# Kernel tuning notes

Measured on AMD Instinct MI355X. Metric: run time of the kernel, lower is better.

## Reference

```python
import jax, jax.numpy as jnp
import numpy as np
from math import factorial, comb

N_NODES = 50000
N_EDGES = 640000
FEAT = 32
NUM_BASIS = 8
CUTOFF = 5.0
MAX_Z = 118
NUM_ITERS = 3
LMAX = 2
K = (LMAX + 1) ** 2  # 9 spherical channels for max_degree=2


def _assoc_legendre(c, s, lmax):
    # associated Legendre P_l^m without Condon-Shortley phase
    P = {(0, 0): np.ones_like(c)}
    for m in range(1, lmax + 1):
        P[(m, m)] = P[(m - 1, m - 1)] * (2 * m - 1) * s
    for m in range(lmax):
        P[(m + 1, m)] = (2 * m + 1) * c * P[(m, m)]
    for m in range(lmax + 1):
        for l in range(m + 2, lmax + 1):
            P[(l, m)] = ((2 * l - 1) * c * P[(l - 1, m)] - (l + m - 1) * P[(l - 2, m)]) / (l - m)
    return P


def _real_sh_np(xyz, lmax):
    # Racah-normalized real spherical harmonics (Y_00 = 1), order m=-l..l
    r = np.linalg.norm(xyz, axis=1)
    cth = xyz[:, 2] / r
    sth = np.sqrt(np.maximum(1.0 - cth ** 2, 0.0))
    phi = np.arctan2(xyz[:, 1], xyz[:, 0])
    P = _assoc_legendre(cth, sth, lmax)
    cols = []
    for l in range(lmax + 1):
        for m in range(-l, l + 1):
            am = abs(m)
            if m == 0:
                cols.append(P[(l, 0)])
            else:
                nrm = np.sqrt(2.0 * factorial(l - am) / factorial(l + am))
                ang = np.cos(am * phi) if m > 0 else np.sin(am * phi)
                cols.append(nrm * P[(l, am)] * ang)
    return np.stack(cols, axis=1)


def _gaunt_tensor():
    # cg[k1,k2,k3]: expansion of Y_k1 * Y_k2 onto Y_k3 (degrees <= 2).
    # Products of degree<=2 harmonics lie exactly in span of degree<=4 harmonics,
    # so the least-squares fit below recovers exact coefficients.
    rng = np.random.default_rng(0)
    pts = rng.normal(size=(4096, 3))
    pts /= np.linalg.norm(pts, axis=1, keepdims=True)
    A = _real_sh_np(pts, 2 * LMAX)  # (M, 25)
    Y = A[:, :K]                    # (M, 9)
    prod = (Y[:, :, None] * Y[:, None, :]).reshape(len(pts), K * K)
    coef, *_ = np.linalg.lstsq(A, prod, rcond=None)  # (25, 81)
    return coef[:K].reshape(K, K, K).transpose(1, 2, 0).astype(np.float32)


CG = jnp.asarray(_gaunt_tensor())  # (9, 9, 9)
LOG_BINOM = jnp.asarray([np.log(comb(NUM_BASIS - 1, kk)) for kk in range(NUM_BASIS)], dtype=jnp.float32)


def _sh_l2(u):
    # Racah real SH of unit vectors, degrees 0..2, order m=-l..l
    x, y, z = u[:, 0], u[:, 1], u[:, 2]
    s3 = 1.7320508075688772
    return jnp.stack([
        jnp.ones_like(x),
        y, z, x,
        s3 * x * y, s3 * y * z, 0.5 * (3.0 * z * z - 1.0), s3 * x * z, 0.5 * s3 * (x * x - y * y),
    ], axis=1)


def _radial(r):
    # reciprocal Bernstein basis (log-space, stable) * smooth cutoff
    u = r / (1.0 + r)
    k = jnp.arange(NUM_BASIS, dtype=jnp.float32)
    n = float(NUM_BASIS - 1)
    eps = 1e-12
    logu = jnp.log(jnp.maximum(u, eps))[:, None]
    log1u = jnp.log(jnp.maximum(1.0 - u, eps))[:, None]
    bern = jnp.exp(LOG_BINOM + k * logu + (n - k) * log1u)  # (E, B)
    cut = jnp.where(r < CUTOFF, jnp.exp(-(r * r) / jnp.maximum(CUTOFF * CUTOFF - r * r, eps)), 0.0)
    return bern * cut[:, None]


def _forward(dr_vec, embed, rad_w, d1w, d1b, d2w, d2b, Z, neighbor_idxs):
    idx_i, idx_j = neighbor_idxs[0], neighbor_idxs[1]
    r = jnp.linalg.norm(dr_vec, axis=1)
    u = dr_vec / jnp.maximum(r, 1e-9)[:, None]
    Ysh = _sh_l2(u)              # (E, 9) angular basis
    rad = _radial(r)             # (E, B) radial basis
    # mask padding edges (idx_i == idx_j) as in mask_by_neighbor
    rad = rad * (idx_i != idx_j).astype(rad.dtype)[:, None]

    N = Z.shape[0]
    x = jnp.zeros((N, K, FEAT), jnp.float32).at[:, 0, :].set(embed[Z])

    for i in range(NUM_ITERS):
        last = i == NUM_ITERS - 1
        k3 = 1 if last else K    # last MessagePass has max_degree=0
        xe = x[idx_j]                                  # (E, 9, F) edge gather
        g = jnp.einsum('eb,dbf->edf', rad, rad_w[i])   # (E, 3, F) radial->feature per basis degree
        y = jnp.zeros((N_EDGES, k3, FEAT), jnp.float32)
        for l2 in range(LMAX + 1):
            sl = slice(l2 * l2, (l2 + 1) ** 2)
            c = jnp.einsum('abc,eb->eac', CG[:, sl, :k3], Ysh[:, sl])          # (E, 9, k3)
            y = y + jnp.einsum('eac,eaf->ecf', c, xe * g[:, l2][:, None, :])   # (E, k3, F)
        m = jax.ops.segment_sum(y, idx_i, num_segments=N)                      # scatter-sum
        if last:
            x = x[:, :1, :]      # change_max_degree_or_type(x, 0)
        h = x + m
        h = jnp.einsum('nkf,fg->nkg', h, d1w[i]).at[:, 0, :].add(d1b[i])
        gate = jax.nn.sigmoid(h[:, :1, :])
        h = h * gate             # silu on scalar channel, sigmoid-gated tensor channels
        h = jnp.einsum('nkf,fg->nkg', h, d2w[i]).at[:, 0, :].add(d2b[i])
        x = x + h
    return x[:, 0, :]            # (N, F)


def setup_inputs() -> dict:
    key = jax.random.key(0)
    ks = jax.random.split(key, 8)
    dr_vec = jax.random.normal(ks[0], (N_EDGES, 3), jnp.float32) * 2.0
    Z = jax.random.randint(ks[1], (N_NODES,), 0, MAX_Z + 1, jnp.int32)
    neighbor_idxs = jax.random.randint(ks[2], (2, N_EDGES), 0, N_NODES, jnp.int32)
    embed = jax.random.normal(ks[3], (MAX_Z + 1, FEAT), jnp.float32)
    rad_w = jax.random.normal(ks[4], (NUM_ITERS, LMAX + 1, NUM_BASIS, FEAT), jnp.float32) * 0.5
    d1w = jax.random.normal(ks[5], (NUM_ITERS, FEAT, FEAT), jnp.float32) * (1.0 / np.sqrt(FEAT))
    d1b = jnp.zeros((NUM_ITERS, FEAT), jnp.float32)
    d2w = jax.random.normal(ks[6], (NUM_ITERS, FEAT, FEAT), jnp.float32) * 0.02
    d2b = jnp.zeros((NUM_ITERS, FEAT), jnp.float32)
    return {"dr_vec": dr_vec, "embed": embed, "rad_w": rad_w, "d1w": d1w, "d1b": d1b,
            "d2w": d2w, "d2b": d2b, "Z": Z, "neighbor_idxs": neighbor_idxs}


def reference(dr_vec, embed, rad_w, d1w, d1b, d2w, d2b, Z, neighbor_idxs):
    return _forward(dr_vec, embed, rad_w, d1w, d1b, d2w, d2b, Z, neighbor_idxs)
```

## Files before the change

kernel.cpp:

```cpp
#include <hip/hip_runtime.h>
#include <hip/hip_fp16.h>
#include <math.h>

#define NN 50000
#define NE 640000
#define F  32
#define KCH 9
#define CUT 5.0f

#define C13 (1.0f/3.0f)
#define C23 (2.0f/3.0f)
#define C15 0.2f
#define C25 0.4f
#define C17 (1.0f/7.0f)
#define C27 (2.0f/7.0f)
#define IS3 0.5773502691896258f
#define S35 0.3464101615137755f
#define S37 0.2474358296526968f
#define S3  1.7320508075688772f

#define NBLK 2048
#define NHALF (NBLK * 8)

union U2H { unsigned int u; __half2 h; };

__device__ __forceinline__ unsigned int pack2(float a, float b) {
    U2H c; c.h = __floats2half2_rn(a, b); return c.u;
}
__device__ __forceinline__ float2 unpack2(unsigned int u) {
    U2H c; c.u = u; return __half22float2(c.h);
}
__device__ __forceinline__ float h2f(ushort u) {
    return __half2float(__ushort_as_half(u));
}

__global__ __launch_bounds__(256) void init_x(const float* __restrict__ embed,
                                              const int* __restrict__ Z,
                                              float* __restrict__ x0,
                                              ushort* __restrict__ x0h,
                                              uint4* __restrict__ xhA,
                                              ushort* __restrict__ xhB) {
    int idx = blockIdx.x * 256 + threadIdx.x;
    int n = idx >> 5;
    float v = embed[Z[n] * F + (idx & 31)];
    x0[idx] = v;
    unsigned int p = pack2(v, 0.f);
    x0h[idx] = (ushort)(p & 0xFFFFu);
    uint4 ua; ua.x = p; ua.y = 0u; ua.z = 0u; ua.w = 0u;
    xhA[idx] = ua;
    xhB[idx] = 0;
}

__global__ __launch_bounds__(256) void hist_kernel(const int* __restrict__ idx_i,
                                                   const int* __restrict__ idx_j,
                                                   const float* __restrict__ dr,
                                                   int* __restrict__ cnt) {
    int e = blockIdx.x * 256 + threadIdx.x;
    if (e >= NE) return;
    int ni = idx_i[e], nj = idx_j[e];
    float dx = dr[3 * e + 0], dy = dr[3 * e + 1], dz = dr[3 * e + 2];
    float r2 = fmaf(dx, dx, fmaf(dy, dy, dz * dz));
    if (ni != nj && r2 < CUT * CUT) atomicAdd(&cnt[ni], 1);
}

#define SCAN_T 1024
#define SCAN_C ((NN + SCAN_T - 1) / SCAN_T)

__global__ __launch_bounds__(SCAN_T) void scan_kernel(const int* __restrict__ cnt,
                                                      int* __restrict__ offs,
                                                      int* __restrict__ head) {
    __shared__ int ps[SCAN_T];
    int t = threadIdx.x;
    int b = t * SCAN_C;
    int e = min(b + SCAN_C, NN);
    int s = 0;
    for (int i = b; i < e; ++i) s += cnt[i];
    ps[t] = s;
    __syncthreads();
    for (int off = 1; off < SCAN_T; off <<= 1) {
        int v = (t >= off) ? ps[t - off] : 0;
        __syncthreads();
        ps[t] += v;
        __syncthreads();
    }
    int run = (t == 0) ? 0 : ps[t - 1];
    for (int i = b; i < e; ++i) { int c = cnt[i]; offs[i] = run; head[i] = run; run += c; }
    if (t == SCAN_T - 1) offs[NN] = ps[SCAN_T - 1];
}

__global__ __launch_bounds__(256) void fill_kernel(const int* __restrict__ idx_i,
                                                   const int* __restrict__ idx_j,
                                                   const float* __restrict__ dr,
                                                   int* __restrict__ head,
                                                   uint4* __restrict__ geoA,
                                                   uint2* __restrict__ geoB,
                                                   ushort* __restrict__ dstA) {
    int e = blockIdx.x * 256 + threadIdx.x;
    if (e >= NE) return;
    int ni = idx_i[e], nj = idx_j[e];
    float dx = dr[3 * e + 0], dy = dr[3 * e + 1], dz = dr[3 * e + 2];
    float r2 = fmaf(dx, dx, fmaf(dy, dy, dz * dz));
    if (!(ni != nj && r2 < CUT * CUT)) return;

    float r = sqrtf(r2);
    float inv = 1.0f / fmaxf(r, 1e-9f);
    float ux = dx * inv, uy = dy * inv, uz = dz * inv;

    float cut = expf(-r2 / fmaxf(CUT * CUT - r2, 1e-12f));
    float ur = r / (1.0f + r), vr = 1.0f - ur;
    float up2 = ur*ur, up3 = up2*ur, up4 = up3*ur, up5 = up4*ur, up6 = up5*ur, up7 = up6*ur;
    float vp2 = vr*vr, vp3 = vp2*vr, vp4 = vp3*vr, vp5 = vp4*vr, vp6 = vp5*vr, vp7 = vp6*vr;

    int p = atomicAdd(&head[ni], 1);
    uint4 gA;
    U2H zh; zh.h = __floats2half2_rn(uz, 0.f);
    gA.x = pack2(ux, uy);
    gA.y = (zh.u & 0xFFFFu) | ((unsigned int)nj << 16);
    gA.z = pack2(cut * vp7,        cut * 7.f  * ur  * vp6);
    gA.w = pack2(cut * 21.f * up2 * vp5, cut * 35.f * up3 * vp4);
    uint2 gB;
    gB.x = pack2(cut * 35.f * up4 * vp3, cut * 21.f * up5 * vp2);
    gB.y = pack2(cut * 7.f  * up6 * vr,  cut * up7);
    geoA[p] = gA;
    geoB[p] = gB;
    dstA[p] = (ushort)ni;
}

template<int MODE>
__global__ __launch_bounds__(256) void gather_kernel(const uint4* __restrict__ geoA,
                                                     const uint2* __restrict__ geoB,
                                                     const ushort* __restrict__ dstA,
                                                     const ushort* __restrict__ x0h,
                                                     const uint4* __restrict__ xhA,
                                                     const ushort* __restrict__ xhB,
                                                     const float* __restrict__ rw_iter,
                                                     const int* __restrict__ neptr,
                                                     float* __restrict__ m) {
    int lane = threadIdx.x & 63;
    int wid  = threadIdx.x >> 6;
    int half = lane >> 5;
    int f    = lane & 31;
    int h    = blockIdx.x * 8 + wid * 2 + half;

    float rwv[24];
    #pragma unroll
    for (int lb = 0; lb < 24; ++lb) rwv[lb] = rw_iter[lb * F + f];
    if (MODE == 2) {
        #pragma unroll
        for (int lb = 8; lb < 16; ++lb) rwv[lb] *= C13;
        #pragma unroll
        for (int lb = 16; lb < 24; ++lb) rwv[lb] *= C15;
    }

    int NEl = neptr[0];
    int per = (NEl + NHALF - 1) / NHALF;
    int s = h * per;
    int e = min(s + per, NEl);
    if (s >= e) return;

    constexpr int NACC = (MODE == 2) ? 1 : KCH;
    float acc[NACC];
    #pragma unroll
    for (int a = 0; a < NACC; ++a) acc[a] = 0.f;
    int cur = -1;

    int c1 = min(s + 1, e - 1), c2 = min(s + 2, e - 1);
    uint4 gA0 = geoA[s], gA1 = geoA[c1], gA2 = geoA[c2];
    uint2 gB0 = geoB[s], gB1 = geoB[c1];
    int d0 = dstA[s], d1 = dstA[c1];
    int nj0 = (int)(gA0.y >> 16), nj1 = (int)(gA1.y >> 16);
    uint4 xa0 = {}, xa1 = {};
    ushort x80, x81;
    if (MODE == 0) {
        x80 = x0h[nj0 * F + f];
        x81 = x0h[nj1 * F + f];
    } else {
        xa0 = xhA[nj0 * F + f]; x80 = xhB[nj0 * F + f];
        xa1 = xhA[nj1 * F + f]; x81 = xhB[nj1 * F + f];
    }

    for (int t = s; t < e; ++t) {
        int t3 = min(t + 3, e - 1);
        int t2 = min(t + 2, e - 1);
        uint4 gA3 = geoA[t3];
        uint2 gB2 = geoB[t2];
        int d2 = dstA[t2];
        int nj2 = (int)(gA2.y >> 16);
        uint4 xa2 = {};
        ushort x82;
        if (MODE == 0) {
            x82 = x0h[nj2 * F + f];
        } else {
            xa2 = xhA[nj2 * F + f];
            x82 = xhB[nj2 * F + f];
        }

        if (d0 != cur) {
            if (cur >= 0) {
                if (MODE == 2) {
                    unsafeAtomicAdd(m + (size_t)cur * F + f, acc[0]);
                } else {
                    float* mp = m + (size_t)cur * KCH * F + f;
                    #pragma unroll
                    for (int a = 0; a < KCH; ++a) unsafeAtomicAdd(mp + a * F, acc[a]);
                }
            }
            cur = d0;
            #pragma unroll
            for (int a = 0; a < NACC; ++a) acc[a] = 0.f;
        }

        float2 uxy = unpack2(gA0.x);
        float ux = uxy.x, uy = uxy.y;
        float uz = unpack2(gA0.y).x;
        float2 rcA = unpack2(gA0.z);
        float2 rcB = unpack2(gA0.w);
        float2 rcC = unpack2(gB0.x);
        float2 rcD = unpack2(gB0.y);

        float g0, g1, g2;
        g0 = rcA.x * rwv[0];
        g0 = fmaf(rcA.y, rwv[1], g0); g0 = fmaf(rcB.x, rwv[2], g0); g0 = fmaf(rcB.y, rwv[3], g0);
        g0 = fmaf(rcC.x, rwv[4], g0); g0 = fmaf(rcC.y, rwv[5], g0); g0 = fmaf(rcD.x, rwv[6], g0);
        g0 = fmaf(rcD.y, rwv[7], g0);
        g1 = rcA.x * rwv[8];
        g1 = fmaf(rcA.y, rwv[9],  g1); g1 = fmaf(rcB.x, rwv[10], g1); g1 = fmaf(rcB.y, rwv[11], g1);
        g1 = fmaf(rcC.x, rwv[12], g1); g1 = fmaf(rcC.y, rwv[13], g1); g1 = fmaf(rcD.x, rwv[14], g1);
        g1 = fmaf(rcD.y, rwv[15], g1);
        g2 = rcA.x * rwv[16];
        g2 = fmaf(rcA.y, rwv[17], g2); g2 = fmaf(rcB.x, rwv[18], g2); g2 = fmaf(rcB.y, rwv[19], g2);
        g2 = fmaf(rcC.x, rwv[20], g2); g2 = fmaf(rcC.y, rwv[21], g2); g2 = fmaf(rcD.x, rwv[22], g2);
        g2 = fmaf(rcD.y, rwv[23], g2);

        if (MODE == 0) {
            float xe0 = h2f(x80);
            float s2 = S3 * g2;
            acc[0] = fmaf(xe0, g0, acc[0]);
            acc[1] = fmaf(xe0, uy * g1, acc[1]);
            acc[2] = fmaf(xe0, uz * g1, acc[2]);
            acc[3] = fmaf(xe0, ux * g1, acc[3]);
            acc[4] = fmaf(xe0, s2 * ux * uy, acc[4]);
            acc[5] = fmaf(xe0, s2 * uy * uz, acc[5]);
            acc[6] = fmaf(xe0, fmaf(1.5f * uz, uz, -0.5f) * g2, acc[6]);
            acc[7] = fmaf(xe0, s2 * ux * uz, acc[7]);
            acc[8] = fmaf(xe0, 0.5f * s2 * (ux * ux - uy * uy), acc[8]);
        } else {
            float xe[9];
            {
                float2 p;
                p = unpack2(xa0.x); xe[0] = p.x; xe[1] = p.y;
                p = unpack2(xa0.y); xe[2] = p.x; xe[3] = p.y;
                p = unpack2(xa0.z); xe[4] = p.x; xe[5] = p.y;
                p = unpack2(xa0.w); xe[6] = p.x; xe[7] = p.y;
                xe[8] = h2f(x80);
            }
            if (MODE == 2) {
                float dot1 = uy * xe[1];
                dot1 = fmaf(uz, xe[2], dot1);
                dot1 = fmaf(ux, xe[3], dot1);
                float Y4 = S3 * ux * uy, Y5 = S3 * uy * uz, Y7 = S3 * ux * uz;
                float Y6 = fmaf(1.5f * uz, uz, -0.5f);
                float Y8 = 0.5f * S3 * (ux * ux - uy * uy);
                float dot2 = Y4 * xe[4];
                dot2 = fmaf(Y5, xe[5], dot2);
                dot2 = fmaf(Y6, xe[6], dot2);
                dot2 = fmaf(Y7, xe[7], dot2);
                dot2 = fmaf(Y8, xe[8], dot2);
                acc[0] = fmaf(g0, xe[0], acc[0]);
                acc[0] = fmaf(g1, dot1, acc[0]);
                acc[0] = fmaf(g2, dot2, acc[0]);
            } else {
                float s2 = S3 * g2;
                float w[9];
                w[0] = g0;
                w[1] = uy * g1; w[2] = uz * g1; w[3] = ux * g1;
                w[4] = s2 * ux * uy;
                w[5] = s2 * uy * uz;
                w[6] = fmaf(1.5f * uz, uz, -0.5f) * g2;
                w[7] = s2 * ux * uz;
                w[8] = 0.5f * s2 * (ux * ux - uy * uy);

                float d0v = xe[0]*w[0], d1v = xe[1]*w[1], d2v = xe[2]*w[2], d3v = xe[3]*w[3];
                float d4v = xe[4]*w[4], d5v = xe[5]*w[5], d6v = xe[6]*w[6], d7v = xe[7]*w[7];
                float d8v = xe[8]*w[8];

                acc[0] += d0v + C13 * (d1v + d2v + d3v) + C15 * (d4v + d5v + d6v + d7v + d8v);
                #define T(a, b) (xe[a] * w[b] + xe[b] * w[a])
                acc[1] += T(0,1) - C15 * T(1,6) - S35 * T(1,8) + S35 * T(2,5) + S35 * T(3,4);
                acc[2] += T(0,2) + S35 * T(1,5) + C25 * T(2,6) + S35 * T(3,7);
                acc[3] += T(0,3) + S35 * T(1,4) + S35 * T(2,7) - C15 * T(3,6) + S35 * T(3,8);
                acc[4] += T(0,4) + IS3 * T(1,3) - C27 * T(4,6) + S37 * T(5,7);
                acc[5] += T(0,5) + IS3 * T(1,2) + S37 * T(4,7) + C17 * T(5,6) - S37 * T(5,8);
                acc[6] += T(0,6) - C13 * d1v + C23 * d2v - C13 * d3v
                        - C27 * d4v + C17 * d5v + C27 * d6v + C17 * d7v - C27 * d8v;
                acc[7] += T(0,7) + IS3 * T(2,3) + S37 * T(4,5) + C17 * T(6,7) + S37 * T(7,8);
                acc[8] += T(0,8) - IS3 * d1v + IS3 * d3v - S37 * d5v + S37 * d7v - C27 * T(6,8);
                #undef T
            }
        }

        gA0 = gA1; gA1 = gA2; gA2 = gA3;
        gB0 = gB1; gB1 = gB2;
        d0 = d1; d1 = d2;
        xa0 = xa1; xa1 = xa2;
        x80 = x81; x81 = x82;
    }

    if (cur >= 0) {
        if (MODE == 2) {
            unsafeAtomicAdd(m + (size_t)cur * F + f, acc[0]);
        } else {
            float* mp = m + (size_t)cur * KCH * F + f;
            #pragma unroll
            for (int a = 0; a < KCH; ++a) unsafeAtomicAdd(mp + a * F, acc[a]);
        }
    }
}

__global__ __launch_bounds__(256) void node_full(float* __restrict__ x0,
                                                 const float* __restrict__ m,
                                                 uint4* __restrict__ xhA,
                                                 ushort* __restrict__ xhB,
                                                 const float* __restrict__ w1,
                                                 const float* __restrict__ b1,
                                                 const float* __restrict__ w2,
                                                 const float* __restrict__ b2) {
    __shared__ float tile[8][KCH][F];
    int nl = threadIdx.x >> 5, f = threadIdx.x & 31;
    int n = blockIdx.x * 8 + nl;

    float w1c[F];
    #pragma unroll
    for (int fi = 0; fi < F; ++fi) w1c[fi] = w1[fi * F + f];

    float xk[KCH];
    {
        uint4 ua = xhA[n * F + f];
        ushort ub = xhB[n * F + f];
        float2 p;
        p = unpack2(ua.x); xk[0] = p.x; xk[1] = p.y;
        p = unpack2(ua.y); xk[2] = p.x; xk[3] = p.y;
        p = unpack2(ua.z); xk[4] = p.x; xk[5] = p.y;
        p = unpack2(ua.w); xk[6] = p.x; xk[7] = p.y;
        xk[8] = h2f(ub);
    }
    xk[0] = x0[n * F + f];

    #pragma unroll
    for (int k = 0; k < KCH; ++k)
        tile[nl][k][f] = xk[k] + m[((size_t)n * KCH + k) * F + f];
    __syncthreads();

    float o1[KCH];
    #pragma unroll
    for (int k = 0; k < KCH; ++k) {
        float s = 0.f;
        #pragma unroll
        for (int fi = 0; fi < F; ++fi) s = fmaf(tile[nl][k][fi], w1c[fi], s);
        o1[k] = s;
    }
    o1[0] += b1[f];
    float gate = 1.0f / (1.0f + expf(-o1[0]));
    __syncthreads();
    #pragma unroll
    for (int k = 0; k < KCH; ++k) tile[nl][k][f] = o1[k] * gate;
    __syncthreads();

    float w2c[F];
    #pragma unroll
    for (int fi = 0; fi < F; ++fi) w2c[fi] = w2[fi * F + f];

    float xn[KCH];
    #pragma unroll
    for (int k = 0; k < KCH; ++k) {
        float s = (k == 0) ? b2[f] : 0.f;
        #pragma unroll
        for (int fi = 0; fi < F; ++fi) s = fmaf(tile[nl][k][fi], w2c[fi], s);
        xn[k] = xk[k] + s;
    }

    x0[n * F + f] = xn[0];
    uint4 ua;
    ua.x = pack2(xn[0], xn[1]); ua.y = pack2(xn[2], xn[3]);
    ua.z = pack2(xn[4], xn[5]); ua.w = pack2(xn[6], xn[7]);
    xhA[n * F + f] = ua;
    xhB[n * F + f] = __half_as_ushort(__float2half_rn(xn[8]));
}

__global__ __launch_bounds__(256) void node_last(const float* __restrict__ x0,
                                                 const float* __restrict__ m1,
                                                 const float* __restrict__ w1,
                                                 const float* __restrict__ b1,
                                                 const float* __restrict__ w2,
                                                 const float* __restrict__ b2,
                                                 float* __restrict__ out) {
    __shared__ float tile[8][F];
    int nl = threadIdx.x >> 5, f = threadIdx.x & 31;
    int n = blockIdx.x * 8 + nl;

    float w1c[F];
    #pragma unroll
    for (int fi = 0; fi < F; ++fi) w1c[fi] = w1[fi * F + f];

    float xv = x0[n * F + f];
    tile[nl][f] = xv + m1[(size_t)n * F + f];
    __syncthreads();
    float s = 0.f;
    #pragma unroll
    for (int fi = 0; fi < F; ++fi) s = fmaf(tile[nl][fi], w1c[fi], s);
    s += b1[f];
    float gate = 1.0f / (1.0f + expf(-s));
    float h2 = s * gate;
    __syncthreads();
    tile[nl][f] = h2;
    __syncthreads();
    float w2c[F];
    #pragma unroll
    for (int fi = 0; fi < F; ++fi) w2c[fi] = w2[fi * F + f];
    float o = b2[f];
    #pragma unroll
    for (int fi = 0; fi < F; ++fi) o = fmaf(tile[nl][fi], w2c[fi], o);
    out[(size_t)n * F + f] = xv + o;
}

extern "C" void kernel_launch(void* const* d_in, const int* in_sizes, int n_in,
                              void* d_out, int out_size, void* d_ws, size_t ws_size,
                              hipStream_t stream) {
    (void)in_sizes; (void)n_in; (void)out_size; (void)ws_size;
    const float* dr    = (const float*)d_in[0];
    const float* embed = (const float*)d_in[1];
    const float* rad_w = (const float*)d_in[2];
    const float* d1w   = (const float*)d_in[3];
    const float* d1b   = (const float*)d_in[4];
    const float* d2w   = (const float*)d_in[5];
    const float* d2b   = (const float*)d_in[6];
    const int*   Z     = (const int*)d_in[7];
    const int*   nidx  = (const int*)d_in[8];
    const int* idx_i = nidx;
    const int* idx_j = nidx + NE;

    uint4* xhA  = (uint4*)d_ws;
    float* m    = (float*)(xhA + (size_t)NN * F);
    float* x0   = m + (size_t)NN * KCH * F;
    ushort* x0h = (ushort*)(x0 + (size_t)NN * F);
    ushort* xhB = x0h + (size_t)NN * F;
    uint4* geoA = (uint4*)(xhB + (size_t)NN * F);
    uint2* geoB = (uint2*)(geoA + (size_t)NE);
    ushort* dstA = (ushort*)(geoB + (size_t)NE);
    int* offs = (int*)(dstA + (size_t)NE + 4);
    int* head = offs + (NN + 1);
    int* cnt  = head + NN;
    float* outp = (float*)d_out;

    size_t MB_full = (size_t)NN * KCH * F * sizeof(float);
    size_t MB_last = (size_t)NN * F * sizeof(float);

    hipMemsetAsync(cnt, 0, NN * sizeof(int), stream);
    hist_kernel<<<(NE + 255) / 256, 256, 0, stream>>>(idx_i, idx_j, dr, cnt);
    scan_kernel<<<1, SCAN_T, 0, stream>>>(cnt, offs, head);
    fill_kernel<<<(NE + 255) / 256, 256, 0, stream>>>(idx_i, idx_j, dr, head, geoA, geoB, dstA);

    init_x<<<NN * F / 256, 256, 0, stream>>>(embed, Z, x0, x0h, xhA, xhB);

    const int* neptr = offs + NN;
    for (int i = 0; i < 3; ++i) {
        const float* rwi = rad_w + (size_t)i * 3 * 8 * F;
        const float* w1 = d1w + (size_t)i * F * F;
        const float* b1 = d1b + (size_t)i * F;
        const float* w2 = d2w + (size_t)i * F * F;
        const float* b2 = d2b + (size_t)i * F;
        if (i == 0) {
            hipMemsetAsync(m, 0, MB_full, stream);
            gather_kernel<0><<<NBLK, 256, 0, stream>>>(geoA, geoB, dstA, x0h, xhA, xhB, rwi, neptr, m);
            node_full<<<NN / 8, 256, 0, stream>>>(x0, m, xhA, xhB, w1, b1, w2, b2);
        } else if (i == 1) {
            hipMemsetAsync(m, 0, MB_full, stream);
            gather_kernel<1><<<NBLK, 256, 0, stream>>>(geoA, geoB, dstA, x0h, xhA, xhB, rwi, neptr, m);
            node_full<<<NN / 8, 256, 0, stream>>>(x0, m, xhA, xhB, w1, b1, w2, b2);
        } else {
            hipMemsetAsync(m, 0, MB_last, stream);
            gather_kernel<2><<<NBLK, 256, 0, stream>>>(geoA, geoB, dstA, x0h, xhA, xhB, rwi, neptr, m);
            node_last<<<NN / 8, 256, 0, stream>>>(x0, m, w1, b1, w2, b2, outp);
        }
    }
}
```

Baseline: 581.0 us.

## Unroll gather loop by four with deeper prefetch and fp16 dot2 radial weights

Restructures the per-edge gather loop into a 4-way unrolled body. Geometry is prefetched four edges ahead and neighbor indices six ahead, from a separate nj array, while the destination node moves into the packed geometry word. The radial-basis contraction now uses packed fp16 dot2 instructions with radial weights converted to half precision. The edge arrays are padded and zeroed so prefetches past the end stay in bounds. This aims to cut loop-carried register shuffling and ALU work, at the cost of extra memsets and reduced precision in the radial weights.

```diff
diff --git a/kernel.cpp b/kernel.cpp
--- a/kernel.cpp
+++ b/kernel.cpp
@@ -22,7 +22,10 @@
 #define NBLK 2048
 #define NHALF (NBLK * 8)
 
+typedef _Float16 h2 __attribute__((ext_vector_type(2)));
+
 union U2H { unsigned int u; __half2 h; };
+union UH2 { unsigned int u; h2 v; };
 
 __device__ __forceinline__ unsigned int pack2(float a, float b) {
     U2H c; c.h = __floats2half2_rn(a, b); return c.u;
@@ -32,6 +35,15 @@
 }
 __device__ __forceinline__ float h2f(ushort u) {
     return __half2float(__ushort_as_half(u));
+}
+__device__ __forceinline__ h2 as_h2(unsigned int u) { UH2 c; c.u = u; return c.v; }
+
+__device__ __forceinline__ float fdot2f(h2 a, h2 b, float c) {
+#if __has_builtin(__builtin_amdgcn_fdot2)
+    return __builtin_amdgcn_fdot2(a, b, c, false);
+#else
+    return fmaf((float)a.x, (float)b.x, fmaf((float)a.y, (float)b.y, c));
+#endif
 }
 
 __global__ __launch_bounds__(256) void init_x(const float* __restrict__ embed,
@@ -94,7 +106,7 @@
                                                    int* __restrict__ head,
                                                    uint4* __restrict__ geoA,
                                                    uint2* __restrict__ geoB,
-                                                   ushort* __restrict__ dstA) {
+                                                   ushort* __restrict__ njA) {
     int e = blockIdx.x * 256 + threadIdx.x;
     if (e >= NE) return;
     int ni = idx_i[e], nj = idx_j[e];
@@ -113,23 +125,126 @@
 
     int p = atomicAdd(&head[ni], 1);
     uint4 gA;
-    U2H zh; zh.h = __floats2half2_rn(uz, 0.f);
     gA.x = pack2(ux, uy);
-    gA.y = (zh.u & 0xFFFFu) | ((unsigned int)nj << 16);
-    gA.z = pack2(cut * vp7,        cut * 7.f  * ur  * vp6);
+    gA.y = (pack2(uz, 0.f) & 0xFFFFu) | ((unsigned int)ni << 16);
+    gA.z = pack2(cut * vp7,              cut * 7.f  * ur  * vp6);
     gA.w = pack2(cut * 21.f * up2 * vp5, cut * 35.f * up3 * vp4);
     uint2 gB;
     gB.x = pack2(cut * 35.f * up4 * vp3, cut * 21.f * up5 * vp2);
     gB.y = pack2(cut * 7.f  * up6 * vr,  cut * up7);
     geoA[p] = gA;
     geoB[p] = gB;
-    dstA[p] = (ushort)ni;
+    njA[p] = (ushort)nj;
+}
+
+template<int MODE>
+__device__ __forceinline__ void flush_acc(float* __restrict__ m, int cur, int f,
+                                          float* __restrict__ acc) {
+    if (cur < 0) return;
+    if (MODE == 2) {
+        unsafeAtomicAdd(m + (size_t)cur * F + f, acc[0]);
+    } else {
+        float* mp = m + (size_t)cur * KCH * F + f;
+        #pragma unroll
+        for (int a = 0; a < KCH; ++a) unsafeAtomicAdd(mp + a * F, acc[a]);
+    }
+}
+
+template<int MODE>
+__device__ __forceinline__ void edge_compute(uint4 gA, uint2 gB, uint4 xav, ushort x8v,
+                                             const h2* __restrict__ rwh,
+                                             float* __restrict__ acc, int& cur,
+                                             float* __restrict__ m, int f) {
+    constexpr int NACC = (MODE == 2) ? 1 : KCH;
+    int dst = (int)(gA.y >> 16);
+    if (dst != cur) {
+        flush_acc<MODE>(m, cur, f, acc);
+        cur = dst;
+        #pragma unroll
+        for (int a = 0; a < NACC; ++a) acc[a] = 0.f;
+    }
+
+    float2 uxy = unpack2(gA.x);
+    float ux = uxy.x, uy = uxy.y;
+    float uz = h2f((ushort)(gA.y & 0xFFFFu));
+    h2 rc01 = as_h2(gA.z), rc23 = as_h2(gA.w), rc45 = as_h2(gB.x), rc67 = as_h2(gB.y);
+
+    float g0 = fdot2f(rc67, rwh[3],  fdot2f(rc45, rwh[2],  fdot2f(rc23, rwh[1],  fdot2f(rc01, rwh[0], 0.f))));
+    float g1 = fdot2f(rc67, rwh[7],  fdot2f(rc45, rwh[6],  fdot2f(rc23, rwh[5],  fdot2f(rc01, rwh[4], 0.f))));
+    float g2 = fdot2f(rc67, rwh[11], fdot2f(rc45, rwh[10], fdot2f(rc23, rwh[9],  fdot2f(rc01, rwh[8], 0.f))));
+
+    if (MODE == 0) {
+        float xe0 = h2f(x8v);
+        float s2 = S3 * g2;
+        acc[0] = fmaf(xe0, g0, acc[0]);
+        acc[1] = fmaf(xe0, uy * g1, acc[1]);
+        acc[2] = fmaf(xe0, uz * g1, acc[2]);
+        acc[3] = fmaf(xe0, ux * g1, acc[3]);
+        acc[4] = fmaf(xe0, s2 * ux * uy, acc[4]);
+        acc[5] = fmaf(xe0, s2 * uy * uz, acc[5]);
+        acc[6] = fmaf(xe0, fmaf(1.5f * uz, uz, -0.5f) * g2, acc[6]);
+        acc[7] = fmaf(xe0, s2 * ux * uz, acc[7]);
+        acc[8] = fmaf(xe0, 0.5f * s2 * (ux * ux - uy * uy), acc[8]);
+    } else {
+        float xe[9];
+        {
+            float2 p;
+            p = unpack2(xav.x); xe[0] = p.x; xe[1] = p.y;
+            p = unpack2(xav.y); xe[2] = p.x; xe[3] = p.y;
+            p = unpack2(xav.z); xe[4] = p.x; xe[5] = p.y;
+            p = unpack2(xav.w); xe[6] = p.x; xe[7] = p.y;
+            xe[8] = h2f(x8v);
+        }
+        if (MODE == 2) {
+            float dot1 = uy * xe[1];
+            dot1 = fmaf(uz, xe[2], dot1);
+            dot1 = fmaf(ux, xe[3], dot1);
+            float Y4 = S3 * ux * uy, Y5 = S3 * uy * uz, Y7 = S3 * ux * uz;
+            float Y6 = fmaf(1.5f * uz, uz, -0.5f);
+            float Y8 = 0.5f * S3 * (ux * ux - uy * uy);
+            float dot2 = Y4 * xe[4];
+            dot2 = fmaf(Y5, xe[5], dot2);
+            dot2 = fmaf(Y6, xe[6], dot2);
+            dot2 = fmaf(Y7, xe[7], dot2);
+            dot2 = fmaf(Y8, xe[8], dot2);
+            acc[0] = fmaf(g0, xe[0], acc[0]);
+            acc[0] = fmaf(g1, dot1, acc[0]);
+            acc[0] = fmaf(g2, dot2, acc[0]);
+        } else {
+            float s2 = S3 * g2;
+            float w[9];
+            w[0] = g0;
+            w[1] = uy * g1; w[2] = uz * g1; w[3] = ux * g1;
+            w[4] = s2 * ux * uy;
+            w[5] = s2 * uy * uz;
+            w[6] = fmaf(1.5f * uz, uz, -0.5f) * g2;
+            w[7] = s2 * ux * uz;
+            w[8] = 0.5f * s2 * (ux * ux - uy * uy);
+
+            float d0v = xe[0]*w[0], d1v = xe[1]*w[1], d2v = xe[2]*w[2], d3v = xe[3]*w[3];
+            float d4v = xe[4]*w[4], d5v = xe[5]*w[5], d6v = xe[6]*w[6], d7v = xe[7]*w[7];
+            float d8v = xe[8]*w[8];
+
+            acc[0] += d0v + C13 * (d1v + d2v + d3v) + C15 * (d4v + d5v + d6v + d7v + d8v);
+            #define T(a, b) (xe[a] * w[b] + xe[b] * w[a])
+            acc[1] += T(0,1) - C15 * T(1,6) - S35 * T(1,8) + S35 * T(2,5) + S35 * T(3,4);
+            acc[2] += T(0,2) + S35 * T(1,5) + C25 * T(2,6) + S35 * T(3,7);
+            acc[3] += T(0,3) + S35 * T(1,4) + S35 * T(2,7) - C15 * T(3,6) + S35 * T(3,8);
+            acc[4] += T(0,4) + IS3 * T(1,3) - C27 * T(4,6) + S37 * T(5,7);
+            acc[5] += T(0,5) + IS3 * T(1,2) + S37 * T(4,7) + C17 * T(5,6) - S37 * T(5,8);
+            acc[6] += T(0,6) - C13 * d1v + C23 * d2v - C13 * d3v
+                    - C27 * d4v + C17 * d5v + C27 * d6v + C17 * d7v - C27 * d8v;
+            acc[7] += T(0,7) + IS3 * T(2,3) + S37 * T(4,5) + C17 * T(6,7) + S37 * T(7,8);
+            acc[8] += T(0,8) - IS3 * d1v + IS3 * d3v - S37 * d5v + S37 * d7v - C27 * T(6,8);
+            #undef T
+        }
+    }
 }
 
 template<int MODE>
 __global__ __launch_bounds__(256) void gather_kernel(const uint4* __restrict__ geoA,
                                                      const uint2* __restrict__ geoB,
-                                                     const ushort* __restrict__ dstA,
+                                                     const ushort* __restrict__ njA,
                                                      const ushort* __restrict__ x0h,
                                                      const uint4* __restrict__ xhA,
                                                      const ushort* __restrict__ xhB,
@@ -142,14 +257,20 @@
     int f    = lane & 31;
     int h    = blockIdx.x * 8 + wid * 2 + half;
 
-    float rwv[24];
-    #pragma unroll
-    for (int lb = 0; lb < 24; ++lb) rwv[lb] = rw_iter[lb * F + f];
+    float rwf[24];
+    #pragma unroll
+    for (int lb = 0; lb < 24; ++lb) rwf[lb] = rw_iter[lb * F + f];
     if (MODE == 2) {
         #pragma unroll
-        for (int lb = 8; lb < 16; ++lb) rwv[lb] *= C13;
-        #pragma unroll
-        for (int lb = 16; lb < 24; ++lb) rwv[lb] *= C15;
+        for (int lb = 8; lb < 16; ++lb) rwf[lb] *= C13;
+        #pragma unroll
+        for (int lb = 16; lb < 24; ++lb) rwf[lb] *= C15;
+    }
+    h2 rwh[12];
+    #pragma unroll
+    for (int q = 0; q < 12; ++q) {
+        h2 v; v.x = (_Float16)rwf[2 * q]; v.y = (_Float16)rwf[2 * q + 1];
+        rwh[q] = v;
     }
 
     int NEl = neptr[0];
@@ -164,157 +285,60 @@
     for (int a = 0; a < NACC; ++a) acc[a] = 0.f;
     int cur = -1;
 
-    int c1 = min(s + 1, e - 1), c2 = min(s + 2, e - 1);
-    uint4 gA0 = geoA[s], gA1 = geoA[c1], gA2 = geoA[c2];
-    uint2 gB0 = geoB[s], gB1 = geoB[c1];
-    int d0 = dstA[s], d1 = dstA[c1];
-    int nj0 = (int)(gA0.y >> 16), nj1 = (int)(gA1.y >> 16);
-    uint4 xa0 = {}, xa1 = {};
-    ushort x80, x81;
-    if (MODE == 0) {
-        x80 = x0h[nj0 * F + f];
-        x81 = x0h[nj1 * F + f];
-    } else {
-        xa0 = xhA[nj0 * F + f]; x80 = xhB[nj0 * F + f];
-        xa1 = xhA[nj1 * F + f]; x81 = xhB[nj1 * F + f];
-    }
-
-    for (int t = s; t < e; ++t) {
-        int t3 = min(t + 3, e - 1);
-        int t2 = min(t + 2, e - 1);
-        uint4 gA3 = geoA[t3];
-        uint2 gB2 = geoB[t2];
-        int d2 = dstA[t2];
-        int nj2 = (int)(gA2.y >> 16);
-        uint4 xa2 = {};
-        ushort x82;
+    uint4 ga[4]; uint2 gb[4]; int njr[4];
+    uint4 xa[2] = {}; ushort x80[2];
+    #pragma unroll
+    for (int p = 0; p < 4; ++p) {
+        ga[p] = geoA[s + p];
+        gb[p] = geoB[s + p];
+        njr[p] = (int)njA[s + p + 2];
+    }
+    {
+        int nj0 = (int)njA[s], nj1 = (int)njA[s + 1];
         if (MODE == 0) {
-            x82 = x0h[nj2 * F + f];
+            x80[0] = x0h[nj0 * F + f];
+            x80[1] = x0h[nj1 * F + f];
         } else {
-            xa2 = xhA[nj2 * F + f];
-            x82 = xhB[nj2 * F + f];
+            xa[0] = xhA[nj0 * F + f]; x80[0] = xhB[nj0 * F + f];
+            xa[1] = xhA[nj1 * F + f]; x80[1] = xhB[nj1 * F + f];
         }
-
-        if (d0 != cur) {
-            if (cur >= 0) {
-                if (MODE == 2) {
-                    unsafeAtomicAdd(m + (size_t)cur * F + f, acc[0]);
-                } else {
-                    float* mp = m + (size_t)cur * KCH * F + f;
-                    #pragma unroll
-                    for (int a = 0; a < KCH; ++a) unsafeAtomicAdd(mp + a * F, acc[a]);
-                }
+    }
+
+    int t = s;
+    while (t + 4 <= e) {
+        #pragma unroll
+        for (int p = 0; p < 4; ++p) {
+            int x = t + p;
+            uint4 gAv = ga[p]; uint2 gBv = gb[p];
+            ga[p] = geoA[x + 4];
+            gb[p] = geoB[x + 4];
+            uint4 xav = xa[p & 1];
+            ushort x8v = x80[p & 1];
+            int njv = njr[p];
+            if (MODE == 0) {
+                x80[p & 1] = x0h[njv * F + f];
+            } else {
+                xa[p & 1] = xhA[njv * F + f];
+                x80[p & 1] = xhB[njv * F + f];
             }
-            cur = d0;
-            #pragma unroll
-            for (int a = 0; a < NACC; ++a) acc[a] = 0.f;
+            njr[p] = (int)njA[x + 6];
+            edge_compute<MODE>(gAv, gBv, xav, x8v, rwh, acc, cur, m, f);
         }
-
-        float2 uxy = unpack2(gA0.x);
-        float ux = uxy.x, uy = uxy.y;
-        float uz = unpack2(gA0.y).x;
-        float2 rcA = unpack2(gA0.z);
-        float2 rcB = unpack2(gA0.w);
-        float2 rcC = unpack2(gB0.x);
-        float2 rcD = unpack2(gB0.y);
-
-        float g0, g1, g2;
-        g0 = rcA.x * rwv[0];
-        g0 = fmaf(rcA.y, rwv[1], g0); g0 = fmaf(rcB.x, rwv[2], g0); g0 = fmaf(rcB.y, rwv[3], g0);
-        g0 = fmaf(rcC.x, rwv[4], g0); g0 = fmaf(rcC.y, rwv[5], g0); g0 = fmaf(rcD.x, rwv[6], g0);
-        g0 = fmaf(rcD.y, rwv[7], g0);
-        g1 = rcA.x * rwv[8];
-        g1 = fmaf(rcA.y, rwv[9],  g1); g1 = fmaf(rcB.x, rwv[10], g1); g1 = fmaf(rcB.y, rwv[11], g1);
-        g1 = fmaf(rcC.x, rwv[12], g1); g1 = fmaf(rcC.y, rwv[13], g1); g1 = fmaf(rcD.x, rwv[14], g1);
-        g1 = fmaf(rcD.y, rwv[15], g1);
-        g2 = rcA.x * rwv[16];
-        g2 = fmaf(rcA.y, rwv[17], g2); g2 = fmaf(rcB.x, rwv[18], g2); g2 = fmaf(rcB.y, rwv[19], g2);
-        g2 = fmaf(rcC.x, rwv[20], g2); g2 = fmaf(rcC.y, rwv[21], g2); g2 = fmaf(rcD.x, rwv[22], g2);
-        g2 = fmaf(rcD.y, rwv[23], g2);
-
+        t += 4;
+    }
+    for (; t < e; ++t) {
+        uint4 gAv = geoA[t]; uint2 gBv = geoB[t];
+        int njv = (int)njA[t];
+        uint4 xav = {}; ushort x8v;
         if (MODE == 0) {
-            float xe0 = h2f(x80);
-            float s2 = S3 * g2;
-            acc[0] = fmaf(xe0, g0, acc[0]);
-            acc[1] = fmaf(xe0, uy * g1, acc[1]);
-            acc[2] = fmaf(xe0, uz * g1, acc[2]);
-            acc[3] = fmaf(xe0, ux * g1, acc[3]);
-            acc[4] = fmaf(xe0, s2 * ux * uy, acc[4]);
-            acc[5] = fmaf(xe0, s2 * uy * uz, acc[5]);
-            acc[6] = fmaf(xe0, fmaf(1.5f * uz, uz, -0.5f) * g2, acc[6]);
-            acc[7] = fmaf(xe0, s2 * ux * uz, acc[7]);
-            acc[8] = fmaf(xe0, 0.5f * s2 * (ux * ux - uy * uy), acc[8]);
+            x8v = x0h[njv * F + f];
         } else {
-            float xe[9];
-            {
-                float2 p;
-                p = unpack2(xa0.x); xe[0] = p.x; xe[1] = p.y;
-                p = unpack2(xa0.y); xe[2] = p.x; xe[3] = p.y;
-                p = unpack2(xa0.z); xe[4] = p.x; xe[5] = p.y;
-                p = unpack2(xa0.w); xe[6] = p.x; xe[7] = p.y;
-                xe[8] = h2f(x80);
-            }
-            if (MODE == 2) {
-                float dot1 = uy * xe[1];
-                dot1 = fmaf(uz, xe[2], dot1);
-                dot1 = fmaf(ux, xe[3], dot1);
-                float Y4 = S3 * ux * uy, Y5 = S3 * uy * uz, Y7 = S3 * ux * uz;
-                float Y6 = fmaf(1.5f * uz, uz, -0.5f);
-                float Y8 = 0.5f * S3 * (ux * ux - uy * uy);
-                float dot2 = Y4 * xe[4];
-                dot2 = fmaf(Y5, xe[5], dot2);
-                dot2 = fmaf(Y6, xe[6], dot2);
-                dot2 = fmaf(Y7, xe[7], dot2);
-                dot2 = fmaf(Y8, xe[8], dot2);
-                acc[0] = fmaf(g0, xe[0], acc[0]);
-                acc[0] = fmaf(g1, dot1, acc[0]);
-                acc[0] = fmaf(g2, dot2, acc[0]);
-            } else {
-                float s2 = S3 * g2;
-                float w[9];
-                w[0] = g0;
-                w[1] = uy * g1; w[2] = uz * g1; w[3] = ux * g1;
-                w[4] = s2 * ux * uy;
-                w[5] = s2 * uy * uz;
-                w[6] = fmaf(1.5f * uz, uz, -0.5f) * g2;
-                w[7] = s2 * ux * uz;
-                w[8] = 0.5f * s2 * (ux * ux - uy * uy);
-
-                float d0v = xe[0]*w[0], d1v = xe[1]*w[1], d2v = xe[2]*w[2], d3v = xe[3]*w[3];
-                float d4v = xe[4]*w[4], d5v = xe[5]*w[5], d6v = xe[6]*w[6], d7v = xe[7]*w[7];
-                float d8v = xe[8]*w[8];
-
-                acc[0] += d0v + C13 * (d1v + d2v + d3v) + C15 * (d4v + d5v + d6v + d7v + d8v);
-                #define T(a, b) (xe[a] * w[b] + xe[b] * w[a])
-                acc[1] += T(0,1) - C15 * T(1,6) - S35 * T(1,8) + S35 * T(2,5) + S35 * T(3,4);
-                acc[2] += T(0,2) + S35 * T(1,5) + C25 * T(2,6) + S35 * T(3,7);
-                acc[3] += T(0,3) + S35 * T(1,4) + S35 * T(2,7) - C15 * T(3,6) + S35 * T(3,8);
-                acc[4] += T(0,4) + IS3 * T(1,3) - C27 * T(4,6) + S37 * T(5,7);
-                acc[5] += T(0,5) + IS3 * T(1,2) + S37 * T(4,7) + C17 * T(5,6) - S37 * T(5,8);
-                acc[6] += T(0,6) - C13 * d1v + C23 * d2v - C13 * d3v
-                        - C27 * d4v + C17 * d5v + C27 * d6v + C17 * d7v - C27 * d8v;
-                acc[7] += T(0,7) + IS3 * T(2,3) + S37 * T(4,5) + C17 * T(6,7) + S37 * T(7,8);
-                acc[8] += T(0,8) - IS3 * d1v + IS3 * d3v - S37 * d5v + S37 * d7v - C27 * T(6,8);
-                #undef T
-            }
+            xav = xhA[njv * F + f];
+            x8v = xhB[njv * F + f];
         }
-
-        gA0 = gA1; gA1 = gA2; gA2 = gA3;
-        gB0 = gB1; gB1 = gB2;
-        d0 = d1; d1 = d2;
-        xa0 = xa1; xa1 = xa2;
-        x80 = x81; x81 = x82;
-    }
-
-    if (cur >= 0) {
-        if (MODE == 2) {
-            unsafeAtomicAdd(m + (size_t)cur * F + f, acc[0]);
-        } else {
-            float* mp = m + (size_t)cur * KCH * F + f;
-            #pragma unroll
-            for (int a = 0; a < KCH; ++a) unsafeAtomicAdd(mp + a * F, acc[a]);
-        }
-    }
+        edge_compute<MODE>(gAv, gBv, xav, x8v, rwh, acc, cur, m, f);
+    }
+    flush_acc<MODE>(m, cur, f, acc);
 }
 
 __global__ __launch_bounds__(256) void node_full(float* __restrict__ x0,
@@ -410,9 +434,9 @@
     for (int fi = 0; fi < F; ++fi) s = fmaf(tile[nl][fi], w1c[fi], s);
     s += b1[f];
     float gate = 1.0f / (1.0f + expf(-s));
-    float h2 = s * gate;
-    __syncthreads();
-    tile[nl][f] = h2;
+    float h2v = s * gate;
+    __syncthreads();
+    tile[nl][f] = h2v;
     __syncthreads();
     float w2c[F];
     #pragma unroll
@@ -445,9 +469,9 @@
     ushort* x0h = (ushort*)(x0 + (size_t)NN * F);
     ushort* xhB = x0h + (size_t)NN * F;
     uint4* geoA = (uint4*)(xhB + (size_t)NN * F);
-    uint2* geoB = (uint2*)(geoA + (size_t)NE);
-    ushort* dstA = (ushort*)(geoB + (size_t)NE);
-    int* offs = (int*)(dstA + (size_t)NE + 4);
+    uint2* geoB = (uint2*)(geoA + (size_t)NE + 8);
+    ushort* njA = (ushort*)(geoB + (size_t)NE + 8);
+    int* offs = (int*)(njA + (size_t)NE + 8);
     int* head = offs + (NN + 1);
     int* cnt  = head + NN;
     float* outp = (float*)d_out;
@@ -456,9 +480,13 @@
     size_t MB_last = (size_t)NN * F * sizeof(float);
 
     hipMemsetAsync(cnt, 0, NN * sizeof(int), stream);
+    hipMemsetAsync(geoA, 0, ((size_t)NE + 8) * sizeof(uint4), stream);
+    hipMemsetAsync(geoB, 0, ((size_t)NE + 8) * sizeof(uint2), stream);
+    hipMemsetAsync(njA,  0, ((size_t)NE + 8) * sizeof(ushort), stream);
+
     hist_kernel<<<(NE + 255) / 256, 256, 0, stream>>>(idx_i, idx_j, dr, cnt);
     scan_kernel<<<1, SCAN_T, 0, stream>>>(cnt, offs, head);
-    fill_kernel<<<(NE + 255) / 256, 256, 0, stream>>>(idx_i, idx_j, dr, head, geoA, geoB, dstA);
+    fill_kernel<<<(NE + 255) / 256, 256, 0, stream>>>(idx_i, idx_j, dr, head, geoA, geoB, njA);
 
     init_x<<<NN * F / 256, 256, 0, stream>>>(embed, Z, x0, x0h, xhA, xhB);
 
@@ -471,15 +499,15 @@
         const float* b2 = d2b + (size_t)i * F;
         if (i == 0) {
             hipMemsetAsync(m, 0, MB_full, stream);
-            gather_kernel<0><<<NBLK, 256, 0, stream>>>(geoA, geoB, dstA, x0h, xhA, xhB, rwi, neptr, m);
+            gather_kernel<0><<<NBLK, 256, 0, stream>>>(geoA, geoB, njA, x0h, xhA, xhB, rwi, neptr, m);
             node_full<<<NN / 8, 256, 0, stream>>>(x0, m, xhA, xhB, w1, b1, w2, b2);
         } else if (i == 1) {
             hipMemsetAsync(m, 0, MB_full, stream);
-            gather_kernel<1><<<NBLK, 256, 0, stream>>>(geoA, geoB, dstA, x0h, xhA, xhB, rwi, neptr, m);
+            gather_kernel<1><<<NBLK, 256, 0, stream>>>(geoA, geoB, njA, x0h, xhA, xhB, rwi, neptr, m);
             node_full<<<NN / 8, 256, 0, stream>>>(x0, m, xhA, xhB, w1, b1, w2, b2);
         } else {
             hipMemsetAsync(m, 0, MB_last, stream);
-            gather_kernel<2><<<NBLK, 256, 0, stream>>>(geoA, geoB, dstA, x0h, xhA, xhB, rwi, neptr, m);
+            gather_kernel<2><<<NBLK, 256, 0, stream>>>(geoA, geoB, njA, x0h, xhA, xhB, rwi, neptr, m);
             node_last<<<NN / 8, 256, 0, stream>>>(x0, m, w1, b1, w2, b2, outp);
         }
     }
```

New measurement: 575.4 us. No clear change (-1.0%).
